# Performance work log

Measured on AMD Instinct MI355X. Metric: run time of the kernel, lower is better.

Reference implementation:

```python
import jax, jax.numpy as jnp
import numpy as np

NEG_SLOPE = 0.2
CONV3_NUM, CONV1_NUM, POLY_NUM = 3, 5, 4
FEAT_DIM = CONV3_NUM * 84 + CONV1_NUM * 12 + POLY_NUM * 12  # 360
DN = ('NCHW', 'OIHW', 'NCHW')


def leaky_relu(x):
    return jnp.where(x >= 0, x, NEG_SLOPE * x)


def conv3x3(x, feat):
    # per-sample dynamic 3x3 conv: feat[:, :81] -> kernel [3,3,3,3], feat[:, 81:84] -> bias
    B = x.shape[0]
    k = feat[:, :81].reshape(B, 3, 3, 3, 3)
    b = feat[:, 81:84]

    def one(xi, ki, bi):
        y = jax.lax.conv_general_dilated(xi[None], ki, (1, 1), 'SAME', dimension_numbers=DN)[0]
        return y + bi[:, None, None]

    return leaky_relu(jax.vmap(one)(x, k, b))


def conv1x1(x, feat):
    B = x.shape[0]
    k = feat[:, :9].reshape(B, 3, 3, 1, 1)
    b = feat[:, 9:12]

    def one(xi, ki, bi):
        y = jax.lax.conv_general_dilated(xi[None], ki, (1, 1), 'VALID', dimension_numbers=DN)[0]
        return y + bi[:, None, None]

    return leaky_relu(jax.vmap(one)(x, k, b))


def conv_stack(x, feature):
    residual = x
    for i in range(CONV3_NUM):
        x = conv3x3(x, feature[:, i * 84:(i + 1) * 84])
    off = CONV3_NUM * 84
    for i in range(CONV1_NUM):
        x = conv1x1(x, feature[:, off + i * 12:off + (i + 1) * 12])
    return residual + x


def att_map(feat, h_mat, w_mat, xc):
    # product over POLY_NUM of (a*h + b*w + c*x + d)
    att = jnp.ones_like(xc)
    for i in range(POLY_NUM):
        a = feat[:, i * 4 + 0].reshape(-1, 1, 1, 1)
        b = feat[:, i * 4 + 1].reshape(-1, 1, 1, 1)
        c = feat[:, i * 4 + 2].reshape(-1, 1, 1, 1)
        d = feat[:, i * 4 + 3].reshape(-1, 1, 1, 1)
        att = att * (a * h_mat + b * w_mat + c * xc + d)
    return att


def apply_attention(x, feature):
    H, W = x.shape[2], x.shape[3]
    h_mat = (jnp.arange(H, dtype=x.dtype) / H).reshape(1, 1, H, 1)
    w_mat = (jnp.arange(W, dtype=x.dtype) / W).reshape(1, 1, 1, W)
    off = CONV3_NUM * 84 + CONV1_NUM * 12
    atts = [att_map(feature[:, off + c * POLY_NUM * 4: off + (c + 1) * POLY_NUM * 4],
                    h_mat, w_mat, x[:, c:c + 1]) for c in range(3)]  # R, G, B
    att = jnp.concatenate(atts, axis=1)
    return x * (1 + att)


def setup_inputs() -> dict:
    key = jax.random.key(0)
    k1, k2, k3 = jax.random.split(key, 3)
    x = jax.random.uniform(k1, (8, 3, 512, 512), dtype=jnp.float32)
    thumb_x = jax.random.uniform(k2, (8, 3, 64, 64), dtype=jnp.float32)
    Wm = jax.random.normal(k3, (3, FEAT_DIM), dtype=jnp.float32) * 0.05
    bm = jnp.zeros((FEAT_DIM,), dtype=jnp.float32)
    return {"x": x, "thumb_x": thumb_x, "Wm": Wm, "bm": bm}


def reference(x, thumb_x, Wm, bm):
    # meta: GAP over thumbnail -> linear -> per-sample hypernetwork features [B, 360]
    feature = jnp.mean(thumb_x, axis=(2, 3)) @ Wm + bm
    x = conv_stack(x, feature)
    x = apply_attention(x, feature)
    thumb = conv_stack(thumb_x, feature)
    thumb = apply_attention(thumb, feature)
    return (x, thumb)
```

## Files before the change

### kernel.cpp

```cpp
#include <hip/hip_runtime.h>


typedef float v2f __attribute__((ext_vector_type(2)));
#define FMA2(a, b, c) __builtin_elementwise_fma((a), (b), (c))

__device__ __forceinline__ v2f leaky2(v2f v) {
    return __builtin_elementwise_max(v, v * 0.2f);
}

__device__ __forceinline__ v2f ldpair(const float* p) {
    v2f r; __builtin_memcpy(&r, p, 8); return r;
}
__device__ __forceinline__ void stpair(float* p, v2f v) {
    __builtin_memcpy(p, &v, 8);
}

constexpr int NCOLS = 73;
constexpr int CSTRA = 23;
constexpr int CHSA  = NCOLS * CSTRA;
constexpr int ASZ   = 3 * CHSA + 4;
constexpr int CSTRB = 21;
constexpr int CHSB  = NCOLS * CSTRB;
constexpr int BSZ   = 3 * CHSB + 4;

__global__ __launch_bounds__(384) void prep_kernel(
    const float* __restrict__ thumb, const float* __restrict__ Wm,
    const float* __restrict__ bm, float* __restrict__ feat)
{
    const int b = blockIdx.x;
    const int t = threadIdx.x;
    const int ch = t >> 7;
    const int l  = t & 127;
    const float4* p = (const float4*)(thumb + (size_t)b * 3 * 4096);
    float s = 0.f;
#pragma unroll
    for (int k = 0; k < 8; ++k) {
        float4 v = p[ch * 1024 + l + k * 128];
        s += v.x + v.y + v.z + v.w;
    }
    __shared__ float red[384];
    red[t] = s;
    __syncthreads();
    for (int off = 64; off > 0; off >>= 1) {
        if (l < off) red[t] += red[t + off];
        __syncthreads();
    }
    if (t < 360) {
        const float sc = 1.f / 4096.f;
        const float m0 = red[0] * sc, m1 = red[128] * sc, m2 = red[256] * sc;
        feat[b * 360 + t] =
            fmaf(m0, Wm[t], fmaf(m1, Wm[360 + t], fmaf(m2, Wm[720 + t], bm[t])));
    }
}

template<int CHS_, int CSTR_>
__device__ __forceinline__ void conv_rows_pk(
    const float* __restrict__ buf, const float* __restrict__ fw,
    int rb, int gx, v2f acc[3][4])
{
    const float b0 = fw[81], b1 = fw[82], b2 = fw[83];
#pragma unroll
    for (int c = 0; c < 4; ++c) {
        v2f i0 = {b0, b0}; v2f i1 = {b1, b1}; v2f i2 = {b2, b2};
        acc[0][c] = i0; acc[1][c] = i1; acc[2][c] = i2;
    }
    const int c0 = (gx < 0) ? 3 : gx + 3;
#pragma unroll
    for (int ich = 0; ich < 3; ++ich) {
        const int base = ich * CHS_ + rb;
#pragma unroll
        for (int dy = 0; dy < 3; ++dy) {
            v2f win[6];
            win[0] = ldpair(&buf[base + c0 * CSTR_ + dy]);
#pragma unroll
            for (int k = 1; k < 6; ++k)
                win[k] = ldpair(&buf[base + (gx + 3 + k) * CSTR_ + dy]);
#pragma unroll
            for (int oc = 0; oc < 3; ++oc) {
                const float w0 = fw[oc * 27 + ich * 9 + dy * 3 + 0];
                const float w1 = fw[oc * 27 + ich * 9 + dy * 3 + 1];
                const float w2 = fw[oc * 27 + ich * 9 + dy * 3 + 2];
                v2f W0 = {w0, w0}; v2f W1 = {w1, w1}; v2f W2 = {w2, w2};
#pragma unroll
                for (int c = 0; c < 4; ++c) {
                    acc[oc][c] = FMA2(win[c], W0,
                                 FMA2(win[c + 1], W1,
                                 FMA2(win[c + 2], W2, acc[oc][c])));
                }
            }
        }
    }
}

__global__ __launch_bounds__(256, 4) void conv_att_kernel(
    const float* __restrict__ x, const float* __restrict__ thumb,
    const float* __restrict__ feat, float* __restrict__ out)
{
    __shared__ float bufA[ASZ];
    __shared__ float bufB[BSZ];

    int id = blockIdx.x;
    const float* src; float* dst; int H, W, b, trow, tcol;
    if (id < 2048) {
        b = id >> 8; const int t = id & 255;
        H = 512; W = 512; trow = (t >> 3) * 16; tcol = (t & 7) * 64;
        src = x; dst = out;
    } else {
        const int i2 = id - 2048;
        b = i2 >> 2; trow = (i2 & 3) * 16; tcol = 0;
        H = 64; W = 64; src = thumb;
        dst = out + (size_t)8 * 3 * 512 * 512;
    }
    const float* fb = feat + b * 360;
    const int tid = threadIdx.x;

    const float* sbg = src + (size_t)b * 3 * H * W;
    float4 stv[4];
#pragma unroll
    for (int i = 0; i < 4; ++i) {
        const int q = tid + 256 * i;
        const int c = q / 352;
        const int rem = q - c * 352;
        const int mr = rem >> 4;
        const int k  = rem & 15;
        const int gr = trow + mr - 3;
        const int gc0 = tcol + 4 * k;
        float4 v = make_float4(0.f, 0.f, 0.f, 0.f);
        if ((unsigned)gr < (unsigned)H)
            v = *(const float4*)&sbg[(size_t)c * H * W + (size_t)gr * W + gc0];
        stv[i] = v;
    }
    const bool has5 = tid < 32;
    float4 st5 = make_float4(0.f, 0.f, 0.f, 0.f);
    if (has5) {
        const int q = tid + 1024;
        const int rem = q - 704;
        const int mr = rem >> 4;
        const int k  = rem & 15;
        const int gr = trow + mr - 3;
        const int gc0 = tcol + 4 * k;
        if ((unsigned)gr < (unsigned)H)
            st5 = *(const float4*)&sbg[(size_t)2 * H * W + (size_t)gr * W + gc0];
    }
    const bool hasH = tid < 132;
    float4 hv = make_float4(0.f, 0.f, 0.f, 0.f);
    int hc = 0, hmr = 0, hside = 0;
    if (hasH) {
        hc = tid / 44;
        const int rem = tid - hc * 44;
        hmr = rem >> 1;
        hside = rem & 1;
        const int gr = trow + hmr - 3;
        const int gc0 = tcol + (hside ? 64 : -4);
        const bool rok = (unsigned)gr < (unsigned)H;
        const float* gp = sbg + (size_t)hc * H * W + (size_t)(rok ? gr : 0) * W;
        if (rok && (unsigned)gc0 <= (unsigned)(W - 4)) {
            hv = *(const float4*)&gp[gc0];
        } else {
            hv.x = (rok && (unsigned)(gc0 + 0) < (unsigned)W) ? gp[gc0 + 0] : 0.f;
            hv.y = (rok && (unsigned)(gc0 + 1) < (unsigned)W) ? gp[gc0 + 1] : 0.f;
            hv.z = (rok && (unsigned)(gc0 + 2) < (unsigned)W) ? gp[gc0 + 2] : 0.f;
            hv.w = (rok && (unsigned)(gc0 + 3) < (unsigned)W) ? gp[gc0 + 3] : 0.f;
        }
    }
#pragma unroll
    for (int i = 0; i < 4; ++i) {
        const int q = tid + 256 * i;
        const int c = q / 352;
        const int rem = q - c * 352;
        const int mr = rem >> 4;
        const int k  = rem & 15;
        float* bp = &bufA[c * CHSA + (4 * k + 4) * CSTRA + mr];
        bp[0] = stv[i].x; bp[CSTRA] = stv[i].y;
        bp[2 * CSTRA] = stv[i].z; bp[3 * CSTRA] = stv[i].w;
    }
    if (has5) {
        const int rem = tid + 1024 - 704;
        const int mr = rem >> 4;
        const int k  = rem & 15;
        float* bp = &bufA[2 * CHSA + (4 * k + 4) * CSTRA + mr];
        bp[0] = st5.x; bp[CSTRA] = st5.y; bp[2 * CSTRA] = st5.z; bp[3 * CSTRA] = st5.w;
    }
    if (hasH) {
        float* bp = &bufA[hc * CHSA + (hside ? 68 : 0) * CSTRA + hmr];
        bp[0] = hv.x; bp[CSTRA] = hv.y; bp[2 * CSTRA] = hv.z; bp[3 * CSTRA] = hv.w;
    }
    if (tid < 66) {
        const int c = tid / 22, mr = tid - c * 22;
        bufA[c * CHSA + 72 * CSTRA + mr] = 0.f;
    } else if (tid < 126) {
        const int t2 = tid - 66;
        const int c = t2 / 20, r = t2 - c * 20;
        bufB[c * CHSB + 72 * CSTRB + r] = 0.f;
    }
    __syncthreads();

    const int s3 = tid >> 4;
    const int gx3 = 4 * (tid & 15);
    v2f res2[3][4];
    if (tid < 128) {
#pragma unroll
        for (int ch = 0; ch < 3; ++ch)
#pragma unroll
            for (int c = 0; c < 4; ++c)
                res2[ch][c] = ldpair(&bufA[ch * CHSA + (gx3 + 4 + c) * CSTRA + (2 * s3 + 3)]);
    }
    {
        const bool act1 = tid < 180;
        int s1, gx1;
        if (tid < 160) { s1 = tid >> 4; gx1 = 4 * (tid & 15); }
        else { const int v = tid - 160; s1 = v >> 1; gx1 = (v & 1) ? 64 : -4; }
        if (act1) {
            v2f acc[3][4];
            conv_rows_pk<CHSA, CSTRA>(bufA, fb, 2 * s1, gx1, acc);
#pragma unroll
            for (int oc = 0; oc < 3; ++oc)
#pragma unroll
                for (int c = 0; c < 4; ++c)
                    stpair(&bufB[oc * CHSB + (gx1 + 4 + c) * CSTRB + 2 * s1],
                           leaky2(acc[oc][c]));
        }
    }
    __syncthreads();

    {
        const bool act2 = tid < 162;
        int s2, gx2;
        if (tid < 144) { s2 = tid >> 4; gx2 = 4 * (tid & 15); }
        else { const int v = tid - 144; s2 = v >> 1; gx2 = (v & 1) ? 64 : -4; }
        if (act2) {
            v2f acc[3][4];
            conv_rows_pk<CHSB, CSTRB>(bufB, fb + 84, 2 * s2, gx2, acc);
#pragma unroll
            for (int oc = 0; oc < 3; ++oc)
#pragma unroll
                for (int c = 0; c < 4; ++c)
                    stpair(&bufA[oc * CHSA + (gx2 + 4 + c) * CSTRA + 2 * s2 + 2],
                           leaky2(acc[oc][c]));
        }
    }
    __syncthreads();

    if (tid < 128) {
        v2f y[3][4];
        {
            v2f acc3[3][4];
            conv_rows_pk<CHSA, CSTRA>(bufA, fb + 168, 2 * s3 + 2, gx3, acc3);
#pragma unroll
            for (int oc = 0; oc < 3; ++oc)
#pragma unroll
                for (int c = 0; c < 4; ++c) y[oc][c] = leaky2(acc3[oc][c]);
        }

#pragma unroll
        for (int lay = 0; lay < 5; ++lay) {
            const float* fw = fb + 252 + lay * 12;
            v2f W0 = {fw[0], fw[0]}; v2f W1 = {fw[1], fw[1]}; v2f W2 = {fw[2], fw[2]};
            v2f W3 = {fw[3], fw[3]}; v2f W4 = {fw[4], fw[4]}; v2f W5 = {fw[5], fw[5]};
            v2f W6 = {fw[6], fw[6]}; v2f W7 = {fw[7], fw[7]}; v2f W8 = {fw[8], fw[8]};
            v2f C0 = {fw[9], fw[9]}; v2f C1 = {fw[10], fw[10]}; v2f C2 = {fw[11], fw[11]};
            v2f z0[4], z1[4], z2[4];
#pragma unroll
            for (int c = 0; c < 4; ++c) {
                z0[c] = FMA2(y[0][c], W0, FMA2(y[1][c], W1, FMA2(y[2][c], W2, C0)));
                z1[c] = FMA2(y[0][c], W3, FMA2(y[1][c], W4, FMA2(y[2][c], W5, C1)));
                z2[c] = FMA2(y[0][c], W6, FMA2(y[1][c], W7, FMA2(y[2][c], W8, C2)));
            }
#pragma unroll
            for (int c = 0; c < 4; ++c) {
                y[0][c] = leaky2(z0[c]);
                y[1][c] = leaky2(z1[c]);
                y[2][c] = leaky2(z2[c]);
            }
        }

        const float invH = 1.f / (float)H;
        const float invW = 1.f / (float)W;
        const int gr0 = trow + 2 * s3;
        v2f h2 = {(float)gr0 * invH, (float)(gr0 + 1) * invH};
        const float wb = (float)(tcol + gx3) * invW;
        const v2f one = {1.f, 1.f};
#pragma unroll
        for (int ch = 0; ch < 3; ++ch) {
            const float* fp = fb + 312 + ch * 16;
            v2f PA0 = {fp[0], fp[0]},  PB0 = {fp[1], fp[1]},  PC0 = {fp[2], fp[2]},  PD0 = {fp[3], fp[3]};
            v2f PA1 = {fp[4], fp[4]},  PB1 = {fp[5], fp[5]},  PC1 = {fp[6], fp[6]},  PD1 = {fp[7], fp[7]};
            v2f PA2 = {fp[8], fp[8]},  PB2 = {fp[9], fp[9]},  PC2 = {fp[10], fp[10]}, PD2 = {fp[11], fp[11]};
            v2f PA3 = {fp[12], fp[12]}, PB3 = {fp[13], fp[13]}, PC3 = {fp[14], fp[14]}, PD3 = {fp[15], fp[15]};
            v2f t0 = FMA2(PA0, h2, PD0);
            v2f t1 = FMA2(PA1, h2, PD1);
            v2f t2 = FMA2(PA2, h2, PD2);
            v2f t3 = FMA2(PA3, h2, PD3);
            v2f o[4];
#pragma unroll
            for (int c = 0; c < 4; ++c) {
                const float wcs = wb + (float)c * invW;
                v2f Wc = {wcs, wcs};
                v2f v = y[ch][c] + res2[ch][c];
                v2f a = FMA2(PB0, Wc, FMA2(PC0, v, t0));
                a = a * FMA2(PB1, Wc, FMA2(PC1, v, t1));
                a = a * FMA2(PB2, Wc, FMA2(PC2, v, t2));
                a = a * FMA2(PB3, Wc, FMA2(PC3, v, t3));
                o[c] = v * (one + a);
            }
            float4 ra = make_float4(o[0].x, o[1].x, o[2].x, o[3].x);
            float4 rb = make_float4(o[0].y, o[1].y, o[2].y, o[3].y);
            float* dp = &dst[((size_t)(b * 3 + ch) * H + gr0) * W + tcol + gx3];
            *(float4*)dp = ra;
            *(float4*)(dp + W) = rb;
        }
    }
}

extern "C" void kernel_launch(void* const* d_in, const int* in_sizes, int n_in,
                              void* d_out, int out_size, void* d_ws, size_t ws_size,
                              hipStream_t stream) {
    const float* x = (const float*)d_in[0];
    const float* thumb = (const float*)d_in[1];
    const float* Wm = (const float*)d_in[2];
    const float* bm = (const float*)d_in[3];
    float* out = (float*)d_out;
    float* feat = (float*)d_ws;

    prep_kernel<<<8, 384, 0, stream>>>(thumb, Wm, bm, feat);
    conv_att_kernel<<<2080, 256, 0, stream>>>(x, thumb, feat, out);
}
```

Baseline: 110.3 us.

## Spread final conv stage over all threads and reuse row-window loads

The third 3x3 conv, the 1x1 stack and the attention epilogue now run on all 256 threads with 2 columns each, instead of 128 threads with 4 columns each. This removes the idle half-block in the last stage. The conv helper now loads two aligned pairs per column and builds the middle-row pair from them, replacing three unaligned 8-byte LDS loads per column. The cost is more per-thread setup and narrower 8-byte global stores in place of float4 stores.

```diff
diff --git a/kernel.cpp b/kernel.cpp
--- a/kernel.cpp
+++ b/kernel.cpp
@@ -53,14 +53,14 @@
     }
 }
 
-template<int CHS_, int CSTR_>
+template<int CHS_, int CSTR_, int NC>
 __device__ __forceinline__ void conv_rows_pk(
     const float* __restrict__ buf, const float* __restrict__ fw,
-    int rb, int gx, v2f acc[3][4])
+    int rb, int gx, v2f acc[3][NC])
 {
     const float b0 = fw[81], b1 = fw[82], b2 = fw[83];
 #pragma unroll
-    for (int c = 0; c < 4; ++c) {
+    for (int c = 0; c < NC; ++c) {
         v2f i0 = {b0, b0}; v2f i1 = {b1, b1}; v2f i2 = {b2, b2};
         acc[0][c] = i0; acc[1][c] = i1; acc[2][c] = i2;
     }
@@ -68,13 +68,17 @@
 #pragma unroll
     for (int ich = 0; ich < 3; ++ich) {
         const int base = ich * CHS_ + rb;
+        v2f p0[NC + 2], p1[NC + 2], pm[NC + 2];
+#pragma unroll
+        for (int k = 0; k < NC + 2; ++k) {
+            const int cc = (k == 0) ? c0 : (gx + 3 + k);
+            p0[k] = ldpair(&buf[base + cc * CSTR_]);
+            p1[k] = ldpair(&buf[base + cc * CSTR_ + 2]);
+            v2f m = {p0[k].y, p1[k].x};
+            pm[k] = m;
+        }
 #pragma unroll
         for (int dy = 0; dy < 3; ++dy) {
-            v2f win[6];
-            win[0] = ldpair(&buf[base + c0 * CSTR_ + dy]);
-#pragma unroll
-            for (int k = 1; k < 6; ++k)
-                win[k] = ldpair(&buf[base + (gx + 3 + k) * CSTR_ + dy]);
 #pragma unroll
             for (int oc = 0; oc < 3; ++oc) {
                 const float w0 = fw[oc * 27 + ich * 9 + dy * 3 + 0];
@@ -82,10 +86,11 @@
                 const float w2 = fw[oc * 27 + ich * 9 + dy * 3 + 2];
                 v2f W0 = {w0, w0}; v2f W1 = {w1, w1}; v2f W2 = {w2, w2};
 #pragma unroll
-                for (int c = 0; c < 4; ++c) {
-                    acc[oc][c] = FMA2(win[c], W0,
-                                 FMA2(win[c + 1], W1,
-                                 FMA2(win[c + 2], W2, acc[oc][c])));
+                for (int c = 0; c < NC; ++c) {
+                    const v2f wa = (dy == 0) ? p0[c]     : (dy == 1) ? pm[c]     : p1[c];
+                    const v2f wb = (dy == 0) ? p0[c + 1] : (dy == 1) ? pm[c + 1] : p1[c + 1];
+                    const v2f wc = (dy == 0) ? p0[c + 2] : (dy == 1) ? pm[c + 2] : p1[c + 2];
+                    acc[oc][c] = FMA2(wa, W0, FMA2(wb, W1, FMA2(wc, W2, acc[oc][c])));
                 }
             }
         }
@@ -195,16 +200,14 @@
     }
     __syncthreads();
 
-    const int s3 = tid >> 4;
-    const int gx3 = 4 * (tid & 15);
-    v2f res2[3][4];
-    if (tid < 128) {
-#pragma unroll
-        for (int ch = 0; ch < 3; ++ch)
-#pragma unroll
-            for (int c = 0; c < 4; ++c)
-                res2[ch][c] = ldpair(&bufA[ch * CHSA + (gx3 + 4 + c) * CSTRA + (2 * s3 + 3)]);
-    }
+    const int s3e = tid >> 5;
+    const int gx3e = 2 * (tid & 31);
+    v2f res2[3][2];
+#pragma unroll
+    for (int ch = 0; ch < 3; ++ch)
+#pragma unroll
+        for (int c = 0; c < 2; ++c)
+            res2[ch][c] = ldpair(&bufA[ch * CHSA + (gx3e + 4 + c) * CSTRA + (2 * s3e + 3)]);
     {
         const bool act1 = tid < 180;
         int s1, gx1;
@@ -212,7 +215,7 @@
         else { const int v = tid - 160; s1 = v >> 1; gx1 = (v & 1) ? 64 : -4; }
         if (act1) {
             v2f acc[3][4];
-            conv_rows_pk<CHSA, CSTRA>(bufA, fb, 2 * s1, gx1, acc);
+            conv_rows_pk<CHSA, CSTRA, 4>(bufA, fb, 2 * s1, gx1, acc);
 #pragma unroll
             for (int oc = 0; oc < 3; ++oc)
 #pragma unroll
@@ -230,7 +233,7 @@
         else { const int v = tid - 144; s2 = v >> 1; gx2 = (v & 1) ? 64 : -4; }
         if (act2) {
             v2f acc[3][4];
-            conv_rows_pk<CHSB, CSTRB>(bufB, fb + 84, 2 * s2, gx2, acc);
+            conv_rows_pk<CHSB, CSTRB, 4>(bufB, fb + 84, 2 * s2, gx2, acc);
 #pragma unroll
             for (int oc = 0; oc < 3; ++oc)
 #pragma unroll
@@ -241,15 +244,15 @@
     }
     __syncthreads();
 
-    if (tid < 128) {
-        v2f y[3][4];
+    {
+        v2f y[3][2];
         {
-            v2f acc3[3][4];
-            conv_rows_pk<CHSA, CSTRA>(bufA, fb + 168, 2 * s3 + 2, gx3, acc3);
+            v2f acc3[3][2];
+            conv_rows_pk<CHSA, CSTRA, 2>(bufA, fb + 168, 2 * s3e + 2, gx3e, acc3);
 #pragma unroll
             for (int oc = 0; oc < 3; ++oc)
 #pragma unroll
-                for (int c = 0; c < 4; ++c) y[oc][c] = leaky2(acc3[oc][c]);
+                for (int c = 0; c < 2; ++c) y[oc][c] = leaky2(acc3[oc][c]);
         }
 
 #pragma unroll
@@ -259,15 +262,15 @@
             v2f W3 = {fw[3], fw[3]}; v2f W4 = {fw[4], fw[4]}; v2f W5 = {fw[5], fw[5]};
             v2f W6 = {fw[6], fw[6]}; v2f W7 = {fw[7], fw[7]}; v2f W8 = {fw[8], fw[8]};
             v2f C0 = {fw[9], fw[9]}; v2f C1 = {fw[10], fw[10]}; v2f C2 = {fw[11], fw[11]};
-            v2f z0[4], z1[4], z2[4];
-#pragma unroll
-            for (int c = 0; c < 4; ++c) {
+            v2f z0[2], z1[2], z2[2];
+#pragma unroll
+            for (int c = 0; c < 2; ++c) {
                 z0[c] = FMA2(y[0][c], W0, FMA2(y[1][c], W1, FMA2(y[2][c], W2, C0)));
                 z1[c] = FMA2(y[0][c], W3, FMA2(y[1][c], W4, FMA2(y[2][c], W5, C1)));
                 z2[c] = FMA2(y[0][c], W6, FMA2(y[1][c], W7, FMA2(y[2][c], W8, C2)));
             }
 #pragma unroll
-            for (int c = 0; c < 4; ++c) {
+            for (int c = 0; c < 2; ++c) {
                 y[0][c] = leaky2(z0[c]);
                 y[1][c] = leaky2(z1[c]);
                 y[2][c] = leaky2(z2[c]);
@@ -276,9 +279,9 @@
 
         const float invH = 1.f / (float)H;
         const float invW = 1.f / (float)W;
-        const int gr0 = trow + 2 * s3;
+        const int gr0 = trow + 2 * s3e;
         v2f h2 = {(float)gr0 * invH, (float)(gr0 + 1) * invH};
-        const float wb = (float)(tcol + gx3) * invW;
+        const float wb = (float)(tcol + gx3e) * invW;
         const v2f one = {1.f, 1.f};
 #pragma unroll
         for (int ch = 0; ch < 3; ++ch) {
@@ -291,9 +294,9 @@
             v2f t1 = FMA2(PA1, h2, PD1);
             v2f t2 = FMA2(PA2, h2, PD2);
             v2f t3 = FMA2(PA3, h2, PD3);
-            v2f o[4];
-#pragma unroll
-            for (int c = 0; c < 4; ++c) {
+            v2f o[2];
+#pragma unroll
+            for (int c = 0; c < 2; ++c) {
                 const float wcs = wb + (float)c * invW;
                 v2f Wc = {wcs, wcs};
                 v2f v = y[ch][c] + res2[ch][c];
@@ -303,11 +306,11 @@
                 a = a * FMA2(PB3, Wc, FMA2(PC3, v, t3));
                 o[c] = v * (one + a);
             }
-            float4 ra = make_float4(o[0].x, o[1].x, o[2].x, o[3].x);
-            float4 rb = make_float4(o[0].y, o[1].y, o[2].y, o[3].y);
-            float* dp = &dst[((size_t)(b * 3 + ch) * H + gr0) * W + tcol + gx3];
-            *(float4*)dp = ra;
-            *(float4*)(dp + W) = rb;
+            v2f ra = {o[0].x, o[1].x};
+            v2f rb2 = {o[0].y, o[1].y};
+            float* dp = &dst[((size_t)(b * 3 + ch) * H + gr0) * W + tcol + gx3e];
+            __builtin_memcpy(dp, &ra, 8);
+            __builtin_memcpy(dp + W, &rb2, 8);
         }
     }
 }
```

Result: faster. 106.5 us (-3.5%).
